# Kernel optimization log

Hardware: AMD Instinct MI355X
Metric: run time of the kernel (lower is better)

## Reference

```python
import jax, jax.numpy as jnp
import numpy as np

N_NODES = 512      # nodes in the original graph
N_SUB = 512        # NodeDeleted -> one subgraph per node
E_SUB = 2097152    # edges in the union-of-subgraphs graph (avg degree 8)
E_ORIG = 8192      # edges in the original graph
IN_DIM = 64
EMB = 64
L = 4
TASKS = 10


def setup_inputs() -> dict:
    key = jax.random.key(0)
    ks = jax.random.split(key, 16)
    NT = N_NODES * N_SUB
    x = jax.random.normal(ks[0], (NT, IN_DIM), jnp.float32)
    # edges stay within a subgraph: global id = subgraph_id * N + local id
    eg = jax.random.randint(ks[1], (E_SUB,), 0, N_SUB)
    src = jax.random.randint(ks[2], (E_SUB,), 0, N_NODES)
    dst = jax.random.randint(ks[3], (E_SUB,), 0, N_NODES)
    edge_index = jnp.stack([eg * N_NODES + src, eg * N_NODES + dst]).astype(jnp.int32)
    original_edge_index = jax.random.randint(ks[4], (2, E_ORIG), 0, N_NODES).astype(jnp.int32)
    subgraph_node_idx = jnp.tile(jnp.arange(N_NODES, dtype=jnp.int32), N_SUB)
    subgraph_batch = jnp.repeat(jnp.arange(N_SUB, dtype=jnp.int32), N_NODES)
    p = lambda k, shape: jax.random.normal(k, shape, jnp.float32) * 0.05
    return dict(
        x=x,
        Wrel=p(ks[5], (L, EMB, IN_DIM)), brel=jnp.zeros((L, EMB), jnp.float32),
        Wroot=p(ks[6], (L, EMB, IN_DIM)),
        bn_gamma=jnp.ones((L, EMB), jnp.float32), bn_beta=jnp.zeros((L, EMB), jnp.float32),
        Wrel_s=p(ks[7], (L, EMB, IN_DIM)), brel_s=jnp.zeros((L, EMB), jnp.float32),
        Wroot_s=p(ks[8], (L, EMB, IN_DIM)),
        bns_gamma=jnp.ones((L, EMB), jnp.float32), bns_beta=jnp.zeros((L, EMB), jnp.float32),
        W1=p(ks[9], (2 * EMB, EMB)), b1=jnp.zeros((2 * EMB,), jnp.float32),
        W2=p(ks[10], (TASKS, 2 * EMB)), b2=jnp.zeros((TASKS,), jnp.float32),
        edge_index=edge_index, original_edge_index=original_edge_index,
        subgraph_node_idx=subgraph_node_idx, subgraph_batch=subgraph_batch,
        num_nodes_int=N_NODES,
    )


def _gconv(h, ei, Wr, br, Wt, n):
    # PyG GraphConv, aggr='add': lin_rel(sum_{j->i} x_j) + lin_root(x_i)
    agg = jax.ops.segment_sum(h[ei[0]], ei[1], num_segments=n)
    return agg @ Wr.T + br + h @ Wt.T


def _bn(h, g, b):
    # BatchNorm1d, training mode: biased batch stats, eps=1e-5
    mu = h.mean(0)
    var = ((h - mu) ** 2).mean(0)
    return (h - mu) * jax.lax.rsqrt(var + 1e-5) * g + b


def _smean(src, idx, n):
    s = jax.ops.segment_sum(src, idx, num_segments=n)
    c = jax.ops.segment_sum(jnp.ones((src.shape[0], 1), src.dtype), idx, num_segments=n)
    return s / jnp.maximum(c, 1.0)


def reference(x, Wrel, brel, Wroot, bn_gamma, bn_beta, Wrel_s, brel_s, Wroot_s,
              bns_gamma, bns_beta, W1, b1, W2, b2,
              edge_index, original_edge_index, subgraph_node_idx, subgraph_batch,
              num_nodes_int):
    N = num_nodes_int
    NT = x.shape[0]
    S = NT // N  # num_subgraphs
    h = x
    for i in range(Wrel.shape[0]):
        h1 = _bn(_gconv(h, edge_index, Wrel[i], brel[i], Wroot[i], NT),
                 bn_gamma[i], bn_beta[i])
        x_sum = _smean(h, subgraph_node_idx, N)              # [N, emb]
        h2 = _bn(_gconv(x_sum, original_edge_index, Wrel_s[i], brel_s[i], Wroot_s[i], N),
                 bns_gamma[i], bns_beta[i])
        h = jax.nn.relu(h1 + jnp.tile(h2, (S, 1)))           # broadcast h2 to every subgraph
    x_nodes = _smean(h, subgraph_node_idx, N)                # [N, emb]
    z = jax.nn.log_softmax(x_nodes, axis=-1)                 # log_softmax BEFORE final MLP (as in source)
    out = jax.nn.relu(z @ W1.T + b1) @ W2.T + b2             # [N, num_tasks]
    return out
```

## Files before the change

kernel.cpp:

```cpp
#include <hip/hip_runtime.h>
#include <math.h>

#define NT 262144
#define NS 512
#define ES 2097152
#define EO 8192
#define NLAYER 4
#define WROW 68
#define BSL 704
#define EREG 8192

typedef short bf16x8 __attribute__((ext_vector_type(8)));
typedef float f32x4 __attribute__((ext_vector_type(4)));

__device__ __forceinline__ void cvt_hilo(const float* v, bf16x8* hi, bf16x8* lo) {
    union U { bf16x8 v; unsigned u[4]; };
    U H, L;
    #pragma unroll
    for (int q = 0; q < 4; q++) {
        float v0 = v[2 * q], v1 = v[2 * q + 1];
        unsigned h01;
        asm("v_cvt_pk_bf16_f32 %0, %1, %2" : "=v"(h01) : "v"(v0), "v"(v1));
        float l0 = v0 - __uint_as_float(h01 << 16);
        float l1 = v1 - __uint_as_float(h01 & 0xffff0000u);
        unsigned l01;
        asm("v_cvt_pk_bf16_f32 %0, %1, %2" : "=v"(l01) : "v"(l0), "v"(l1));
        H.u[q] = h01; L.u[q] = l01;
    }
    *hi = H.v; *lo = L.v;
}

__global__ __launch_bounds__(256) void bucket_kernel(const int* __restrict__ ei,
        int* __restrict__ gcur, unsigned* __restrict__ rbuf) {
    __shared__ int lcnt[512];
    __shared__ int lcur[512];
    int p = blockIdx.x;
    int g = p & 7;
    int base = p * 4096;
    int tid = threadIdx.x;
    for (int t = tid; t < 512; t += 256) lcnt[t] = 0;
    __syncthreads();
    int subs[16];
    unsigned recs[16];
    #pragma unroll
    for (int j = 0; j < 16; j++) {
        int e = base + j * 256 + tid;
        int d = ei[ES + e];
        int srcl = ei[e] & 511;
        subs[j] = d >> 9;
        recs[j] = (unsigned)srcl | ((unsigned)(d & 511) << 16);
        atomicAdd(&lcnt[subs[j]], 1);
    }
    __syncthreads();
    for (int t = tid; t < 512; t += 256) {
        int c = lcnt[t];
        lcur[t] = c ? atomicAdd(&gcur[g * 512 + t], c) : 0;
    }
    __syncthreads();
    #pragma unroll
    for (int j = 0; j < 16; j++) {
        int s = subs[j];
        int pos = atomicAdd(&lcur[s], 1);
        if (pos < BSL) rbuf[((size_t)s * 8 + g) * BSL + pos] = recs[j];
    }
}

__global__ __launch_bounds__(512) void csr_sub_kernel(const int* __restrict__ gcur,
        const unsigned* __restrict__ rbuf, int* __restrict__ rowptr,
        unsigned short* __restrict__ ebuf) {
    __shared__ int sdeg[512];
    __shared__ int sscan[512];
    __shared__ int scur[512];
    __shared__ unsigned short erow[EREG];
    __shared__ int scnt[8];
    int s = blockIdx.x;
    int t = threadIdx.x;
    sdeg[t] = 0;
    if (t < 8) scnt[t] = min(gcur[t * 512 + s], BSL);
    unsigned* e32 = (unsigned*)erow;
    #pragma unroll
    for (int j = 0; j < 8; j++) e32[j * 512 + t] = 0x02000200u;
    __syncthreads();
    for (int g = 0; g < 8; g++) {
        int cg = scnt[g];
        const unsigned* rb = rbuf + ((size_t)s * 8 + g) * BSL;
        for (int i = t; i < cg; i += 512) atomicAdd(&sdeg[rb[i] >> 16], 1);
    }
    __syncthreads();
    int pdeg = (sdeg[t] + 3) & ~3;
    sscan[t] = pdeg;
    __syncthreads();
    for (int off = 1; off < 512; off <<= 1) {
        int x = (t >= off) ? sscan[t - off] : 0;
        __syncthreads();
        sscan[t] += x;
        __syncthreads();
    }
    int excl = sscan[t] - pdeg;
    scur[t] = excl;
    rowptr[s * 513 + t] = s * EREG + excl;
    if (t == 511) rowptr[s * 513 + 512] = s * EREG + sscan[511];
    __syncthreads();
    for (int g = 0; g < 8; g++) {
        int cg = scnt[g];
        const unsigned* rb = rbuf + ((size_t)s * 8 + g) * BSL;
        for (int i = t; i < cg; i += 512) {
            unsigned rec = rb[i];
            int pos = atomicAdd(&scur[rec >> 16], 1);
            erow[pos] = (unsigned short)(rec & 511);
        }
    }
    __syncthreads();
    uint4* eo = (uint4*)(ebuf + (size_t)s * EREG);
    const uint4* ei4 = (const uint4*)erow;
    eo[t] = ei4[t];
    eo[t + 512] = ei4[t + 512];
}

__global__ void small_csr_kernel(const int* __restrict__ oei, int* __restrict__ rowptrS,
                                 int* __restrict__ srcsS,
                                 const float* __restrict__ Wrel_s,
                                 const float* __restrict__ Wroot_s,
                                 float* __restrict__ WrT, float* __restrict__ WtT) {
    __shared__ int sdeg[NS];
    __shared__ int scur[NS];
    int t = threadIdx.x;
    if (t < NS) sdeg[t] = 0;
    __syncthreads();
    for (int e = t; e < EO; e += 1024) atomicAdd(&sdeg[oei[EO + e]], 1);
    __syncthreads();
    int myv = (t < NS) ? sdeg[t] : 0;
    __syncthreads();
    for (int off = 1; off < NS; off <<= 1) {
        int x = (t >= off && t < NS) ? sdeg[t - off] : 0;
        __syncthreads();
        if (t < NS) sdeg[t] += x;
        __syncthreads();
    }
    if (t < NS) {
        int excl = sdeg[t] - myv;
        rowptrS[t] = excl;
        scur[t] = excl;
        if (t == 0) rowptrS[NS] = EO;
    }
    __syncthreads();
    for (int e = t; e < EO; e += 1024) {
        int d = oei[EO + e];
        int pos = atomicAdd(&scur[d], 1);
        srcsS[pos] = oei[e];
    }
    for (int idx = t; idx < NLAYER * 4096; idx += 1024) {
        int layer = idx >> 12;
        int rem = idx & 4095;
        int cc = rem >> 6, kk = rem & 63;
        WrT[layer * 4096 + kk * 64 + cc] = Wrel_s[idx];
        WtT[layer * 4096 + kk * 64 + cc] = Wroot_s[idx];
    }
}

__global__ __launch_bounds__(512, 2) void gconv_sub_kernel(
    const float* __restrict__ hsrc,
    const float* __restrict__ h2,
    const float* __restrict__ stB, const float* __restrict__ stS,
    const float* __restrict__ gB, const float* __restrict__ bB,
    const float* __restrict__ gS, const float* __restrict__ bS,
    int mode,
    const int* __restrict__ rowptr, const unsigned short* __restrict__ ebuf,
    const float* __restrict__ Wr, const float* __restrict__ Wt,
    const float* __restrict__ br,
    float* __restrict__ hout, float* __restrict__ stats,
    const float* __restrict__ xsumIn, const int* __restrict__ rowptrS,
    const int* __restrict__ srcsS, const float* __restrict__ WrT,
    const float* __restrict__ WtT, const float* __restrict__ brS,
    float* __restrict__ h2out, float* __restrict__ statsS)
{
    extern __shared__ char smem[];
    int tid = threadIdx.x;

    float* Wn = (float*)smem;
    float* bnp = Wn + 513 * WROW;

    int p = blockIdx.x;
    int sub = p;
    int w = tid >> 6;
    int l = tid & 63;
    int cl = l & 15;
    int kg = l >> 4;
    int kg8 = kg * 8;
    int half = w >> 2;
    int m = w & 3;

    if (mode) {
        if (tid < 64) {
            int c = tid;
            float sb = 0.f, qb = 0.f, ss = 0.f, qs = 0.f;
            for (int r2 = 0; r2 < 32; r2++) {
                sb += stB[r2 * 128 + c];
                qb += stB[r2 * 128 + 64 + c];
                ss += stS[r2 * 128 + c];
                qs += stS[r2 * 128 + 64 + c];
            }
            float muB = sb * (1.f / 262144.f);
            float varB = qb * (1.f / 262144.f) - muB * muB;
            float scB = gB[c] * rsqrtf(varB + 1e-5f);
            bnp[c] = scB;
            bnp[64 + c] = bB[c] - muB * scB;
            float muS = ss * (1.f / 512.f);
            float varS = qs * (1.f / 512.f) - muS * muS;
            float scS = gS[c] * rsqrtf(varS + 1e-5f);
            bnp[128 + c] = scS;
            bnp[192 + c] = bS[c] - muS * scS;
        }
        __syncthreads();
    }

    const float* srcbase = hsrc + (size_t)sub * 512 * 64;
    for (int idx = tid; idx < 512 * 16; idx += 512) {
        int r = idx >> 4;
        int c4 = (idx & 15) * 4;
        float4 a = *(const float4*)(srcbase + r * 64 + c4);
        if (mode) {
            float4 b = *(const float4*)(h2 + r * 64 + c4);
            float4 sB4 = *(const float4*)(bnp + c4);
            float4 hB4 = *(const float4*)(bnp + 64 + c4);
            float4 sS4 = *(const float4*)(bnp + 128 + c4);
            float4 hS4 = *(const float4*)(bnp + 192 + c4);
            a.x = fmaxf(a.x * sB4.x + hB4.x + b.x * sS4.x + hS4.x, 0.f);
            a.y = fmaxf(a.y * sB4.y + hB4.y + b.y * sS4.y + hS4.y, 0.f);
            a.z = fmaxf(a.z * sB4.z + hB4.z + b.z * sS4.z + hS4.z, 0.f);
            a.w = fmaxf(a.w * sB4.w + hB4.w + b.w * sS4.w + hS4.w, 0.f);
        }
        *(float4*)(Wn + r * WROW + c4) = a;
    }
    if (tid < WROW) Wn[512 * WROW + tid] = 0.f;

    bf16x8 Bh[16], Bl[16];
    float bias0, bias1, bias2, bias3;
    #pragma unroll
    for (int c = 0; c < 4; c++) {
        int col = c * 16 + cl;
        #pragma unroll
        for (int ch = 0; ch < 4; ch++) {
            const float* mat = (ch < 2) ? Wr : Wt;
            int k = (ch & 1) * 32 + kg8;
            float vv[8];
            *(float4*)vv = *(const float4*)(mat + col * 64 + k);
            *(float4*)(vv + 4) = *(const float4*)(mat + col * 64 + k + 4);
            cvt_hilo(vv, &Bh[c * 4 + ch], &Bl[c * 4 + ch]);
        }
    }
    bias0 = br[cl];
    bias1 = br[16 + cl];
    bias2 = br[32 + cl];
    bias3 = br[48 + cl];

    const uint2* ebuf2 = (const uint2*)ebuf;
    __syncthreads();

#define GATH1(qv) { \
        const float* pp = Wn + (qv) * WROW + kg8; \
        float4 tg0 = *(const float4*)(pp); \
        float4 tg1 = *(const float4*)(pp + 4); \
        float4 tg2 = *(const float4*)(pp + 32); \
        float4 tg3 = *(const float4*)(pp + 36); \
        a0.x += tg0.x; a0.y += tg0.y; a0.z += tg0.z; a0.w += tg0.w; \
        a1.x += tg1.x; a1.y += tg1.y; a1.z += tg1.z; a1.w += tg1.w; \
        a2.x += tg2.x; a2.y += tg2.y; a2.z += tg2.z; a2.w += tg2.w; \
        a3.x += tg3.x; a3.y += tg3.y; a3.z += tg3.z; a3.w += tg3.w; \
    }

#define DO_CHUNK(g0h, g1h, ch) { \
        float gg[8]; \
        *(float4*)gg = g0h; *(float4*)(gg + 4) = g1h; \
        bf16x8 ah, al; \
        cvt_hilo(gg, &ah, &al); \
        acc0 = __builtin_amdgcn_mfma_f32_16x16x32_bf16(ah, Bh[0 * 4 + ch], acc0, 0, 0, 0); \
        acc1 = __builtin_amdgcn_mfma_f32_16x16x32_bf16(ah, Bh[1 * 4 + ch], acc1, 0, 0, 0); \
        acc2 = __builtin_amdgcn_mfma_f32_16x16x32_bf16(ah, Bh[2 * 4 + ch], acc2, 0, 0, 0); \
        acc3 = __builtin_amdgcn_mfma_f32_16x16x32_bf16(ah, Bh[3 * 4 + ch], acc3, 0, 0, 0); \
        acc0 = __builtin_amdgcn_mfma_f32_16x16x32_bf16(al, Bh[0 * 4 + ch], acc0, 0, 0, 0); \
        acc1 = __builtin_amdgcn_mfma_f32_16x16x32_bf16(al, Bh[1 * 4 + ch], acc1, 0, 0, 0); \
        acc2 = __builtin_amdgcn_mfma_f32_16x16x32_bf16(al, Bh[2 * 4 + ch], acc2, 0, 0, 0); \
        acc3 = __builtin_amdgcn_mfma_f32_16x16x32_bf16(al, Bh[3 * 4 + ch], acc3, 0, 0, 0); \
        acc0 = __builtin_amdgcn_mfma_f32_16x16x32_bf16(ah, Bl[0 * 4 + ch], acc0, 0, 0, 0); \
        acc1 = __builtin_amdgcn_mfma_f32_16x16x32_bf16(ah, Bl[1 * 4 + ch], acc1, 0, 0, 0); \
        acc2 = __builtin_amdgcn_mfma_f32_16x16x32_bf16(ah, Bl[2 * 4 + ch], acc2, 0, 0, 0); \
        acc3 = __builtin_amdgcn_mfma_f32_16x16x32_bf16(ah, Bl[3 * 4 + ch], acc3, 0, 0, 0); \
    }

    float s0 = 0.f, s1 = 0.f, s2 = 0.f, s3 = 0.f;
    float q0s = 0.f, q1s = 0.f, q2s = 0.f, q3s = 0.f;

    for (int tt = 0; tt < 4; tt++) {
        int tile = half * 4 + tt;
        int nb = sub * 512 + tile * 64;
        int row = tile * 64 + m * 16 + cl;
        int rpb = sub * 513;
        int e0q = rowptr[rpb + row] >> 2;
        int e1q = rowptr[rpb + row + 1] >> 2;

        float4 a0 = make_float4(0.f, 0.f, 0.f, 0.f);
        float4 a1 = a0, a2 = a0, a3 = a0;
        uint2 rr = make_uint2(0u, 0u);
        int u = e0q;
        if (u < e1q) rr = ebuf2[u];
        while (u < e1q) {
            uint2 cur = rr;
            ++u;
            if (u < e1q) rr = ebuf2[u];
            unsigned q0 = cur.x & 0xffffu;
            unsigned q1 = cur.x >> 16;
            unsigned q2 = cur.y & 0xffffu;
            unsigned q3 = cur.y >> 16;
            GATH1(q0);
            GATH1(q1);
            GATH1(q2);
            GATH1(q3);
        }

        const float* wrow = Wn + (size_t)(tile * 64 + m * 16 + cl) * WROW + kg8;
        float4 r0 = *(const float4*)(wrow);
        float4 r1 = *(const float4*)(wrow + 4);
        float4 r2 = *(const float4*)(wrow + 32);
        float4 r3 = *(const float4*)(wrow + 36);

        f32x4 acc0, acc1, acc2, acc3;
        #pragma unroll
        for (int j = 0; j < 4; j++) {
            acc0[j] = bias0; acc1[j] = bias1; acc2[j] = bias2; acc3[j] = bias3;
        }
        DO_CHUNK(a0, a1, 0);
        DO_CHUNK(a2, a3, 1);
        DO_CHUNK(r0, r1, 2);
        DO_CHUNK(r2, r3, 3);

        int node0 = nb + m * 16 + kg * 4;
        #pragma unroll
        for (int j = 0; j < 4; j++) {
            float v0 = acc0[j], v1 = acc1[j], v2 = acc2[j], v3 = acc3[j];
            size_t rowb = (size_t)(node0 + j) * 64;
            hout[rowb + cl] = v0;
            hout[rowb + 16 + cl] = v1;
            hout[rowb + 32 + cl] = v2;
            hout[rowb + 48 + cl] = v3;
            s0 += v0; q0s += v0 * v0;
            s1 += v1; q1s += v1 * v1;
            s2 += v2; q2s += v2 * v2;
            s3 += v3; q3s += v3 * v3;
        }
    }

    s0 += __shfl_xor(s0, 16, 64); s0 += __shfl_xor(s0, 32, 64);
    s1 += __shfl_xor(s1, 16, 64); s1 += __shfl_xor(s1, 32, 64);
    s2 += __shfl_xor(s2, 16, 64); s2 += __shfl_xor(s2, 32, 64);
    s3 += __shfl_xor(s3, 16, 64); s3 += __shfl_xor(s3, 32, 64);
    q0s += __shfl_xor(q0s, 16, 64); q0s += __shfl_xor(q0s, 32, 64);
    q1s += __shfl_xor(q1s, 16, 64); q1s += __shfl_xor(q1s, 32, 64);
    q2s += __shfl_xor(q2s, 16, 64); q2s += __shfl_xor(q2s, 32, 64);
    q3s += __shfl_xor(q3s, 16, 64); q3s += __shfl_xor(q3s, 32, 64);
    if (kg == 0) {
        int rep = p & 31;
        atomicAdd(&stats[rep * 128 + cl], s0);
        atomicAdd(&stats[rep * 128 + 16 + cl], s1);
        atomicAdd(&stats[rep * 128 + 32 + cl], s2);
        atomicAdd(&stats[rep * 128 + 48 + cl], s3);
        atomicAdd(&stats[rep * 128 + 64 + cl], q0s);
        atomicAdd(&stats[rep * 128 + 80 + cl], q1s);
        atomicAdd(&stats[rep * 128 + 96 + cl], q2s);
        atomicAdd(&stats[rep * 128 + 112 + cl], q3s);
    }

    if (w == 0) {
        int c = l;
        float agg = 0.f;
        int e0 = rowptrS[p], e1 = rowptrS[p + 1];
        for (int e = e0; e < e1; e++) agg += xsumIn[srcsS[e] * 64 + c];
        float own = xsumIn[p * 64 + c];
        float o = brS[c];
        #pragma unroll 4
        for (int k = 0; k < 64; k++) {
            float ak = __shfl(agg, k, 64);
            float hk = __shfl(own, k, 64);
            o += WrT[k * 64 + c] * ak + WtT[k * 64 + c] * hk;
        }
        h2out[p * 64 + c] = o;
        int rep = p & 31;
        atomicAdd(&statsS[rep * 128 + c], o);
        atomicAdd(&statsS[rep * 128 + 64 + c], o * o);
    }
#undef GATH1
#undef DO_CHUNK
}

__global__ __launch_bounds__(1024) void xsum_kernel(
    const float* __restrict__ hsrc, const float* __restrict__ h2,
    const float* __restrict__ stB, const float* __restrict__ stS,
    const float* __restrict__ gB, const float* __restrict__ bB,
    const float* __restrict__ gS, const float* __restrict__ bS,
    int mode, float* __restrict__ xsum)
{
    __shared__ float bnp[256];
    __shared__ float red[16][64];
    int t = threadIdx.x;
    if (mode) {
        if (t < 64) {
            int c = t;
            float sb = 0.f, qb = 0.f, ss = 0.f, qs = 0.f;
            for (int r2 = 0; r2 < 32; r2++) {
                sb += stB[r2 * 128 + c];
                qb += stB[r2 * 128 + 64 + c];
                ss += stS[r2 * 128 + c];
                qs += stS[r2 * 128 + 64 + c];
            }
            float muB = sb * (1.f / 262144.f);
            float varB = qb * (1.f / 262144.f) - muB * muB;
            float scB = gB[c] * rsqrtf(varB + 1e-5f);
            bnp[c] = scB;
            bnp[64 + c] = bB[c] - muB * scB;
            float muS = ss * (1.f / 512.f);
            float varS = qs * (1.f / 512.f) - muS * muS;
            float scS = gS[c] * rsqrtf(varS + 1e-5f);
            bnp[128 + c] = scS;
            bnp[192 + c] = bS[c] - muS * scS;
        }
        __syncthreads();
    }

    int w = t >> 6;
    int l = t & 63;
    int c4 = (l & 15) * 4;
    int r = l >> 4;
    int n = blockIdx.x;

    float bx = 0.f, by = 0.f, bz = 0.f, bw = 0.f;
    float4 sB = make_float4(1.f, 1.f, 1.f, 1.f);
    float4 hB = make_float4(0.f, 0.f, 0.f, 0.f);
    if (mode) {
        sB = *(const float4*)(bnp + c4);
        hB = *(const float4*)(bnp + 64 + c4);
        float4 sS = *(const float4*)(bnp + 128 + c4);
        float4 hS = *(const float4*)(bnp + 192 + c4);
        float4 b2 = *(const float4*)(h2 + n * 64 + c4);
        bx = b2.x * sS.x + hS.x;
        by = b2.y * sS.y + hS.y;
        bz = b2.z * sS.z + hS.z;
        bw = b2.w * sS.w + hS.w;
    }

    float4 acc = make_float4(0.f, 0.f, 0.f, 0.f);
    #pragma unroll
    for (int j = 0; j < 8; j++) {
        int si = w * 32 + j * 4 + r;
        size_t base = (size_t)(si * 512 + n) * 64 + c4;
        float4 a = *(const float4*)(hsrc + base);
        float4 v;
        if (mode) {
            v.x = fmaxf(a.x * sB.x + hB.x + bx, 0.f);
            v.y = fmaxf(a.y * sB.y + hB.y + by, 0.f);
            v.z = fmaxf(a.z * sB.z + hB.z + bz, 0.f);
            v.w = fmaxf(a.w * sB.w + hB.w + bw, 0.f);
        } else {
            v = a;
        }
        acc.x += v.x; acc.y += v.y; acc.z += v.z; acc.w += v.w;
    }
    acc.x += __shfl_xor(acc.x, 16, 64); acc.y += __shfl_xor(acc.y, 16, 64);
    acc.z += __shfl_xor(acc.z, 16, 64); acc.w += __shfl_xor(acc.w, 16, 64);
    acc.x += __shfl_xor(acc.x, 32, 64); acc.y += __shfl_xor(acc.y, 32, 64);
    acc.z += __shfl_xor(acc.z, 32, 64); acc.w += __shfl_xor(acc.w, 32, 64);
    if (l < 16) {
        red[w][c4 + 0] = acc.x;
        red[w][c4 + 1] = acc.y;
        red[w][c4 + 2] = acc.z;
        red[w][c4 + 3] = acc.w;
    }
    __syncthreads();
    if (t < 64) {
        float tot = 0.f;
        #pragma unroll
        for (int ww = 0; ww < 16; ww++) tot += red[ww][t];
        xsum[n * 64 + t] = tot * (1.f / 512.f);
    }
}

__global__ void head_kernel(const float* __restrict__ xs, const float* __restrict__ W1,
                            const float* __restrict__ b1, const float* __restrict__ W2,
                            const float* __restrict__ b2, float* __restrict__ out) {
    __shared__ float z[64];
    __shared__ float hid[128];
    int t = threadIdx.x;
    int n = blockIdx.x;
    if (t < 64) {
        float v = xs[n * 64 + t];
        float m = v;
        for (int off = 32; off >= 1; off >>= 1) m = fmaxf(m, __shfl_xor(m, off, 64));
        float e = expf(v - m);
        float s = e;
        for (int off = 32; off >= 1; off >>= 1) s += __shfl_xor(s, off, 64);
        z[t] = v - m - logf(s);
    }
    __syncthreads();
    {
        float acc = b1[t];
        const float* wrow = W1 + t * 64;
        #pragma unroll 8
        for (int k = 0; k < 64; k++) acc += z[k] * wrow[k];
        hid[t] = fmaxf(acc, 0.f);
    }
    __syncthreads();
    if (t < 10) {
        float o = b2[t];
        const float* wrow = W2 + t * 128;
        #pragma unroll 8
        for (int j = 0; j < 128; j++) o += hid[j] * wrow[j];
        out[n * 10 + t] = o;
    }
}

extern "C" void kernel_launch(void* const* d_in, const int* in_sizes, int n_in,
                              void* d_out, int out_size, void* d_ws, size_t ws_size,
                              hipStream_t stream) {
    const float* x       = (const float*)d_in[0];
    const float* Wrel    = (const float*)d_in[1];
    const float* brel    = (const float*)d_in[2];
    const float* Wroot   = (const float*)d_in[3];
    const float* bn_g    = (const float*)d_in[4];
    const float* bn_b    = (const float*)d_in[5];
    const float* Wrel_s  = (const float*)d_in[6];
    const float* brel_s  = (const float*)d_in[7];
    const float* Wroot_s = (const float*)d_in[8];
    const float* bns_g   = (const float*)d_in[9];
    const float* bns_b   = (const float*)d_in[10];
    const float* W1      = (const float*)d_in[11];
    const float* b1      = (const float*)d_in[12];
    const float* W2      = (const float*)d_in[13];
    const float* b2      = (const float*)d_in[14];
    const int* ei        = (const int*)d_in[15];
    const int* oei       = (const int*)d_in[16];
    float* out = (float*)d_out;

    char* ws = (char*)d_ws;
    size_t off = 0;
    auto alloc = [&](size_t bytes) -> void* {
        void* p = ws + off;
        off = (off + bytes + 255) & ~(size_t)255;
        return p;
    };
    float* h1    = (float*)alloc((size_t)NT * 64 * 4);
    float* xsum  = (float*)alloc(NS * 64 * 4);
    float* h2buf = (float*)alloc((size_t)2 * NS * 64 * 4);
    float* stats = (float*)alloc(NLAYER * 2 * 4096 * 4);
    int* rowptr  = (int*)alloc((size_t)NS * 513 * 4);
    int* gcur    = (int*)alloc(8 * 512 * 4);
    unsigned short* ebuf = (unsigned short*)alloc((size_t)NS * EREG * 2);
    int* rowptrS = (int*)alloc(513 * 4);
    int* srcsS   = (int*)alloc(EO * 4);
    float* wrTs  = (float*)alloc(NLAYER * 4096 * 4);
    float* wtTs  = (float*)alloc(NLAYER * 4096 * 4);
    unsigned* rbuf = (unsigned*)h1;
    (void)ws_size; (void)in_sizes; (void)n_in; (void)out_size;

    hipMemsetAsync(gcur, 0, 8 * 512 * 4, stream);
    hipMemsetAsync(stats, 0, (size_t)NLAYER * 2 * 4096 * 4, stream);

    bucket_kernel<<<ES / 4096, 256, 0, stream>>>(ei, gcur, rbuf);
    csr_sub_kernel<<<NS, 512, 0, stream>>>(gcur, rbuf, rowptr, ebuf);
    small_csr_kernel<<<1, 1024, 0, stream>>>(oei, rowptrS, srcsS,
                                             Wrel_s, Wroot_s, wrTs, wtTs);

    const size_t SMEM = (513 * WROW + 256) * 4;

    for (int i = 0; i < NLAYER; i++) {
        int mode = (i > 0);
        const float* hsrc = mode ? h1 : x;
        const float* h2R = h2buf + (size_t)((i - 1) & 1) * NS * 64;
        float* h2W = h2buf + (size_t)(i & 1) * NS * 64;
        const float* stPB = stats + (i - 1) * 8192;
        const float* stPS = stPB + 4096;
        const float* gBp = bn_g + (i - 1) * 64;
        const float* bBp = bn_b + (i - 1) * 64;
        const float* gSp = bns_g + (i - 1) * 64;
        const float* bSp = bns_b + (i - 1) * 64;
        float* stB = stats + i * 8192;
        float* stS = stB + 4096;

        xsum_kernel<<<NS, 1024, 0, stream>>>(hsrc, h2R, stPB, stPS, gBp, bBp, gSp, bSp,
                                             mode, xsum);
        gconv_sub_kernel<<<NS, 512, SMEM, stream>>>(hsrc, h2R, stPB, stPS,
            gBp, bBp, gSp, bSp, mode, rowptr, ebuf,
            Wrel + i * 4096, Wroot + i * 4096, brel + i * 64, h1, stB,
            xsum, rowptrS, srcsS,
            wrTs + i * 4096, wtTs + i * 4096, brel_s + i * 64, h2W, stS);
    }
    {
        const float* stPB = stats + 3 * 8192;
        const float* stPS = stPB + 4096;
        const float* h2R = h2buf + (size_t)(3 & 1) * NS * 64;
        xsum_kernel<<<NS, 1024, 0, stream>>>(h1, h2R, stPB, stPS,
            bn_g + 3 * 64, bn_b + 3 * 64, bns_g + 3 * 64, bns_b + 3 * 64, 1, xsum);
    }
    head_kernel<<<NS, 128, 0, stream>>>(xsum, W1, b1, W2, b2, out);
}
```

Baseline: 554.5 us.

## Store intermediate node features in fp16 and parallelize subgraph-level conv across block

The per-node pre-BN activations h1 are now written and read as fp16 instead of fp32. This halves the dominant HBM traffic of the gconv and xsum kernels across all layers. Separately, the small original-graph GraphConv tail, previously run by a single wavefront, is split across all eight waves using shared-memory partial sums. The trade-off is reduced precision in the stored activations. BN statistics are still accumulated from fp32 values before rounding, so normalization uses slightly different values than those stored.

Measured after the change: 482.0 us. 13.1% less time.

```diff
diff --git a/kernel.cpp b/kernel.cpp
--- a/kernel.cpp
+++ b/kernel.cpp
@@ -12,6 +12,8 @@
 
 typedef short bf16x8 __attribute__((ext_vector_type(8)));
 typedef float f32x4 __attribute__((ext_vector_type(4)));
+typedef _Float16 half8 __attribute__((ext_vector_type(8)));
+typedef _Float16 half4v __attribute__((ext_vector_type(4)));
 
 __device__ __forceinline__ void cvt_hilo(const float* v, bf16x8* hi, bf16x8* lo) {
     union U { bf16x8 v; unsigned u[4]; };
@@ -159,7 +161,8 @@
 }
 
 __global__ __launch_bounds__(512, 2) void gconv_sub_kernel(
-    const float* __restrict__ hsrc,
+    const float* __restrict__ xsrc,
+    const _Float16* __restrict__ h1prev,
     const float* __restrict__ h2,
     const float* __restrict__ stB, const float* __restrict__ stS,
     const float* __restrict__ gB, const float* __restrict__ bB,
@@ -168,7 +171,7 @@
     const int* __restrict__ rowptr, const unsigned short* __restrict__ ebuf,
     const float* __restrict__ Wr, const float* __restrict__ Wt,
     const float* __restrict__ br,
-    float* __restrict__ hout, float* __restrict__ stats,
+    _Float16* __restrict__ hout, float* __restrict__ stats,
     const float* __restrict__ xsumIn, const int* __restrict__ rowptrS,
     const int* __restrict__ srcsS, const float* __restrict__ WrT,
     const float* __restrict__ WtT, const float* __restrict__ brS,
@@ -214,23 +217,44 @@
         __syncthreads();
     }
 
-    const float* srcbase = hsrc + (size_t)sub * 512 * 64;
-    for (int idx = tid; idx < 512 * 16; idx += 512) {
-        int r = idx >> 4;
-        int c4 = (idx & 15) * 4;
-        float4 a = *(const float4*)(srcbase + r * 64 + c4);
-        if (mode) {
-            float4 b = *(const float4*)(h2 + r * 64 + c4);
-            float4 sB4 = *(const float4*)(bnp + c4);
-            float4 hB4 = *(const float4*)(bnp + 64 + c4);
-            float4 sS4 = *(const float4*)(bnp + 128 + c4);
-            float4 hS4 = *(const float4*)(bnp + 192 + c4);
-            a.x = fmaxf(a.x * sB4.x + hB4.x + b.x * sS4.x + hS4.x, 0.f);
-            a.y = fmaxf(a.y * sB4.y + hB4.y + b.y * sS4.y + hS4.y, 0.f);
-            a.z = fmaxf(a.z * sB4.z + hB4.z + b.z * sS4.z + hS4.z, 0.f);
-            a.w = fmaxf(a.w * sB4.w + hB4.w + b.w * sS4.w + hS4.w, 0.f);
-        }
-        *(float4*)(Wn + r * WROW + c4) = a;
+    if (mode) {
+        int r0w = tid >> 3;
+        int c8 = (tid & 7) * 8;
+        float4 sB0 = *(const float4*)(bnp + c8);
+        float4 sB1 = *(const float4*)(bnp + c8 + 4);
+        float4 hB0 = *(const float4*)(bnp + 64 + c8);
+        float4 hB1 = *(const float4*)(bnp + 64 + c8 + 4);
+        float4 sS0 = *(const float4*)(bnp + 128 + c8);
+        float4 sS1 = *(const float4*)(bnp + 128 + c8 + 4);
+        float4 hS0 = *(const float4*)(bnp + 192 + c8);
+        float4 hS1 = *(const float4*)(bnp + 192 + c8 + 4);
+        const _Float16* hb = h1prev + (size_t)sub * 512 * 64;
+        #pragma unroll
+        for (int k = 0; k < 8; k++) {
+            int r = r0w + k * 64;
+            half8 hv = *(const half8*)(hb + r * 64 + c8);
+            float4 b0 = *(const float4*)(h2 + r * 64 + c8);
+            float4 b1 = *(const float4*)(h2 + r * 64 + c8 + 4);
+            float4 o0, o1;
+            o0.x = fmaxf((float)hv[0] * sB0.x + hB0.x + b0.x * sS0.x + hS0.x, 0.f);
+            o0.y = fmaxf((float)hv[1] * sB0.y + hB0.y + b0.y * sS0.y + hS0.y, 0.f);
+            o0.z = fmaxf((float)hv[2] * sB0.z + hB0.z + b0.z * sS0.z + hS0.z, 0.f);
+            o0.w = fmaxf((float)hv[3] * sB0.w + hB0.w + b0.w * sS0.w + hS0.w, 0.f);
+            o1.x = fmaxf((float)hv[4] * sB1.x + hB1.x + b1.x * sS1.x + hS1.x, 0.f);
+            o1.y = fmaxf((float)hv[5] * sB1.y + hB1.y + b1.y * sS1.y + hS1.y, 0.f);
+            o1.z = fmaxf((float)hv[6] * sB1.z + hB1.z + b1.z * sS1.z + hS1.z, 0.f);
+            o1.w = fmaxf((float)hv[7] * sB1.w + hB1.w + b1.w * sS1.w + hS1.w, 0.f);
+            *(float4*)(Wn + r * WROW + c8) = o0;
+            *(float4*)(Wn + r * WROW + c8 + 4) = o1;
+        }
+    } else {
+        const float* srcbase = xsrc + (size_t)sub * 512 * 64;
+        for (int idx = tid; idx < 512 * 16; idx += 512) {
+            int r = idx >> 4;
+            int c4 = (idx & 15) * 4;
+            float4 a = *(const float4*)(srcbase + r * 64 + c4);
+            *(float4*)(Wn + r * WROW + c4) = a;
+        }
     }
     if (tid < WROW) Wn[512 * WROW + tid] = 0.f;
 
@@ -339,10 +363,10 @@
         for (int j = 0; j < 4; j++) {
             float v0 = acc0[j], v1 = acc1[j], v2 = acc2[j], v3 = acc3[j];
             size_t rowb = (size_t)(node0 + j) * 64;
-            hout[rowb + cl] = v0;
-            hout[rowb + 16 + cl] = v1;
-            hout[rowb + 32 + cl] = v2;
-            hout[rowb + 48 + cl] = v3;
+            hout[rowb + cl] = (_Float16)v0;
+            hout[rowb + 16 + cl] = (_Float16)v1;
+            hout[rowb + 32 + cl] = (_Float16)v2;
+            hout[rowb + 48 + cl] = (_Float16)v3;
             s0 += v0; q0s += v0 * v0;
             s1 += v1; q1s += v1 * v1;
             s2 += v2; q2s += v2 * v2;
@@ -370,30 +394,50 @@
         atomicAdd(&stats[rep * 128 + 112 + cl], q3s);
     }
 
-    if (w == 0) {
-        int c = l;
-        float agg = 0.f;
+    __syncthreads();
+    {
+        float* aggP = Wn;
+        float* ownF = Wn + 512;
+        float* oP   = Wn + 576;
         int e0 = rowptrS[p], e1 = rowptrS[p + 1];
-        for (int e = e0; e < e1; e++) agg += xsumIn[srcsS[e] * 64 + c];
-        float own = xsumIn[p * 64 + c];
-        float o = brS[c];
-        #pragma unroll 4
-        for (int k = 0; k < 64; k++) {
-            float ak = __shfl(agg, k, 64);
-            float hk = __shfl(own, k, 64);
-            o += WrT[k * 64 + c] * ak + WtT[k * 64 + c] * hk;
-        }
-        h2out[p * 64 + c] = o;
-        int rep = p & 31;
-        atomicAdd(&statsS[rep * 128 + c], o);
-        atomicAdd(&statsS[rep * 128 + 64 + c], o * o);
+        float ap = 0.f;
+        for (int e = e0 + w; e < e1; e += 8) ap += xsumIn[srcsS[e] * 64 + l];
+        aggP[w * 64 + l] = ap;
+        if (w == 0) ownF[l] = xsumIn[p * 64 + l];
+        __syncthreads();
+        if (tid < 64) {
+            float s = 0.f;
+            #pragma unroll
+            for (int ww = 0; ww < 8; ww++) s += aggP[ww * 64 + tid];
+            aggP[tid] = s;
+        }
+        __syncthreads();
+        int c = tid & 63, kc = tid >> 6;
+        float op = 0.f;
+        #pragma unroll
+        for (int kk = 0; kk < 8; kk++) {
+            int k = kc * 8 + kk;
+            op += WrT[k * 64 + c] * aggP[k] + WtT[k * 64 + c] * ownF[k];
+        }
+        oP[kc * 64 + c] = op;
+        __syncthreads();
+        if (tid < 64) {
+            float o = brS[tid];
+            #pragma unroll
+            for (int kk = 0; kk < 8; kk++) o += oP[kk * 64 + tid];
+            h2out[p * 64 + tid] = o;
+            int rep = p & 31;
+            atomicAdd(&statsS[rep * 128 + tid], o);
+            atomicAdd(&statsS[rep * 128 + 64 + tid], o * o);
+        }
     }
 #undef GATH1
 #undef DO_CHUNK
 }
 
 __global__ __launch_bounds__(1024) void xsum_kernel(
-    const float* __restrict__ hsrc, const float* __restrict__ h2,
+    const float* __restrict__ xsrc, const _Float16* __restrict__ h1prev,
+    const float* __restrict__ h2,
     const float* __restrict__ stB, const float* __restrict__ stS,
     const float* __restrict__ gB, const float* __restrict__ bB,
     const float* __restrict__ gS, const float* __restrict__ bS,
@@ -452,15 +496,15 @@
     for (int j = 0; j < 8; j++) {
         int si = w * 32 + j * 4 + r;
         size_t base = (size_t)(si * 512 + n) * 64 + c4;
-        float4 a = *(const float4*)(hsrc + base);
         float4 v;
         if (mode) {
-            v.x = fmaxf(a.x * sB.x + hB.x + bx, 0.f);
-            v.y = fmaxf(a.y * sB.y + hB.y + by, 0.f);
-            v.z = fmaxf(a.z * sB.z + hB.z + bz, 0.f);
-            v.w = fmaxf(a.w * sB.w + hB.w + bw, 0.f);
+            half4v a = *(const half4v*)(h1prev + base);
+            v.x = fmaxf((float)a[0] * sB.x + hB.x + bx, 0.f);
+            v.y = fmaxf((float)a[1] * sB.y + hB.y + by, 0.f);
+            v.z = fmaxf((float)a[2] * sB.z + hB.z + bz, 0.f);
+            v.w = fmaxf((float)a[3] * sB.w + hB.w + bw, 0.f);
         } else {
-            v = a;
+            v = *(const float4*)(xsrc + base);
         }
         acc.x += v.x; acc.y += v.y; acc.z += v.z; acc.w += v.w;
     }
@@ -546,7 +590,7 @@
         off = (off + bytes + 255) & ~(size_t)255;
         return p;
     };
-    float* h1    = (float*)alloc((size_t)NT * 64 * 4);
+    _Float16* h1b = (_Float16*)alloc((size_t)NT * 64 * 2);
     float* xsum  = (float*)alloc(NS * 64 * 4);
     float* h2buf = (float*)alloc((size_t)2 * NS * 64 * 4);
     float* stats = (float*)alloc(NLAYER * 2 * 4096 * 4);
@@ -557,7 +601,7 @@
     int* srcsS   = (int*)alloc(EO * 4);
     float* wrTs  = (float*)alloc(NLAYER * 4096 * 4);
     float* wtTs  = (float*)alloc(NLAYER * 4096 * 4);
-    unsigned* rbuf = (unsigned*)h1;
+    unsigned* rbuf = (unsigned*)h1b;
     (void)ws_size; (void)in_sizes; (void)n_in; (void)out_size;
 
     hipMemsetAsync(gcur, 0, 8 * 512 * 4, stream);
@@ -572,7 +616,6 @@
 
     for (int i = 0; i < NLAYER; i++) {
         int mode = (i > 0);
-        const float* hsrc = mode ? h1 : x;
         const float* h2R = h2buf + (size_t)((i - 1) & 1) * NS * 64;
         float* h2W = h2buf + (size_t)(i & 1) * NS * 64;
         const float* stPB = stats + (i - 1) * 8192;
@@ -584,11 +627,11 @@
         float* stB = stats + i * 8192;
         float* stS = stB + 4096;
 
-        xsum_kernel<<<NS, 1024, 0, stream>>>(hsrc, h2R, stPB, stPS, gBp, bBp, gSp, bSp,
-                                             mode, xsum);
-        gconv_sub_kernel<<<NS, 512, SMEM, stream>>>(hsrc, h2R, stPB, stPS,
+        xsum_kernel<<<NS, 1024, 0, stream>>>(x, h1b, h2R, stPB, stPS,
+                                             gBp, bBp, gSp, bSp, mode, xsum);
+        gconv_sub_kernel<<<NS, 512, SMEM, stream>>>(x, h1b, h2R, stPB, stPS,
             gBp, bBp, gSp, bSp, mode, rowptr, ebuf,
-            Wrel + i * 4096, Wroot + i * 4096, brel + i * 64, h1, stB,
+            Wrel + i * 4096, Wroot + i * 4096, brel + i * 64, h1b, stB,
             xsum, rowptrS, srcsS,
             wrTs + i * 4096, wtTs + i * 4096, brel_s + i * 64, h2W, stS);
     }
@@ -596,7 +639,7 @@
         const float* stPB = stats + 3 * 8192;
         const float* stPS = stPB + 4096;
         const float* h2R = h2buf + (size_t)(3 & 1) * NS * 64;
-        xsum_kernel<<<NS, 1024, 0, stream>>>(h1, h2R, stPB, stPS,
+        xsum_kernel<<<NS, 1024, 0, stream>>>(x, h1b, h2R, stPB, stPS,
             bn_g + 3 * 64, bn_b + 3 * 64, bns_g + 3 * 64, bns_b + 3 * 64, 1, xsum);
     }
     head_kernel<<<NS, 128, 0, stream>>>(xsum, W1, b1, W2, b2, out);
```
